# Kernel tuning notes

Hardware: AMD Instinct MI355X
Metric: run time of the kernel (lower is better)

## Reference

```python
import jax, jax.numpy as jnp
import numpy as np

C = 256          # in_channels == out_channels
L = 131072       # sequence length (multiple of BL)
BL = 64          # dilation == sliding-attention block length
CQ = C // 2      # q/k channels (r1=2)
CV = C // 2      # v channels (r2=2)
ALPHA = 1.0
EPS_IN = 1e-5    # InstanceNorm eps


def setup_inputs() -> dict:
    key = jax.random.key(0)
    ks = jax.random.split(key, 16)
    s = 0.05
    return {
        "x": jax.random.normal(ks[0], (1, C, L), jnp.float32),
        "f": jax.random.normal(ks[1], (1, C, L), jnp.float32),
        "mask": jnp.ones((1, 1, L), jnp.float32),
        # ConvFeedForward: Conv1d(C, C, 3, padding=BL, dilation=BL)
        "Wff": jax.random.normal(ks[2], (C, C, 3), jnp.float32) * s,
        "bff": jax.random.normal(ks[3], (C,), jnp.float32) * s,
        # AttLayer 1x1 convs
        "Wq": jax.random.normal(ks[4], (CQ, C), jnp.float32) * s,
        "bq": jax.random.normal(ks[5], (CQ,), jnp.float32) * s,
        "Wk": jax.random.normal(ks[6], (CQ, C), jnp.float32) * s,
        "bk": jax.random.normal(ks[7], (CQ,), jnp.float32) * s,
        "Wv": jax.random.normal(ks[8], (CV, C), jnp.float32) * s,
        "bv": jax.random.normal(ks[9], (CV,), jnp.float32) * s,
        "Wo": jax.random.normal(ks[10], (C, CV), jnp.float32) * s,
        "bo": jax.random.normal(ks[11], (C,), jnp.float32) * s,
        # AttModule.conv_1x1
        "Wc": jax.random.normal(ks[12], (C, C), jnp.float32) * s,
        "bc": jax.random.normal(ks[13], (C,), jnp.float32) * s,
    }


def _conv1x1(W, b, x):  # x: (B, Cin, L)
    return jnp.einsum('oc,bcl->bol', W, x) + b[None, :, None]


def _forward(x, f, mask, Wff, bff, Wq, bq, Wk, bk, Wv, bv, Wo, bo, Wc, bc):
    # --- ConvFeedForward: dilated conv + ReLU (same-length output) ---
    out = jax.lax.conv_general_dilated(
        x, Wff, window_strides=(1,), padding=[(BL, BL)], rhs_dilation=(BL,),
        dimension_numbers=('NCH', 'OIH', 'NCH')) + bff[None, :, None]
    out = jax.nn.relu(out)  # (1, C, L)

    # --- InstanceNorm1d (affine=False, biased var) ---
    mu = out.mean(axis=-1, keepdims=True)
    var = out.var(axis=-1, keepdims=True)
    xn = (out - mu) * jax.lax.rsqrt(var + EPS_IN)

    # --- AttLayer (sliding_att, decoder: value from f) ---
    q = _conv1x1(Wq, bq, xn)   # (1, CQ, L)
    k = _conv1x1(Wk, bk, xn)   # (1, CQ, L)
    v = _conv1x1(Wv, bv, f)    # (1, CV, L)

    nb = L // BL
    half = BL // 2
    pm = mask[:, 0:1, :]                         # (1,1,L) padding mask
    # pad halo of BL//2 zeros on each side of k, v, padding_mask
    kp = jnp.pad(k, ((0, 0), (0, 0), (half, half)))
    vp = jnp.pad(v, ((0, 0), (0, 0), (half, half)))
    mp = jnp.pad(pm, ((0, 0), (0, 0), (half, half)))
    # window index: block i sees [i*BL, i*BL + 2*BL) of the padded sequence
    idx = jnp.arange(nb)[:, None] * BL + jnp.arange(2 * BL)[None, :]  # (nb, 2BL)
    kw = kp[:, :, idx]   # (1, CQ, nb, 2BL)
    vw = vp[:, :, idx]   # (1, CV, nb, 2BL)
    mw = mp[:, 0, idx]   # (1, nb, 2BL)

    # window mask: query i attends keys [i, i+BL) within the 2BL window
    d = jnp.arange(2 * BL)[None, :] - jnp.arange(BL)[:, None]
    wm = ((d >= 0) & (d < BL)).astype(x.dtype)          # (BL, 2BL)
    fm = wm[None, None] * mw[:, :, None, :]             # (1, nb, BL, 2BL)

    qb = q.reshape(1, CQ, nb, BL)
    energy = jnp.einsum('bcnl,bcnm->bnlm', qb, kw) / np.sqrt(CQ).astype(x.dtype)
    att = jax.nn.softmax(energy + jnp.log(fm + 1e-6), axis=-1) * fm
    ov = jnp.einsum('bcnm,bnlm->bcnl', vw, att)         # (1, CV, nb, BL)
    oo = jnp.einsum('oc,bcnl->bonl', Wo, jax.nn.relu(ov)) + bo[None, :, None, None]
    att_out = oo.reshape(1, C, L) * pm                  # (1, C, L)

    # --- scaled residual + 1x1 conv + (dropout=identity) + masked residual ---
    h = ALPHA * att_out + out
    h = _conv1x1(Wc, bc, h)
    return (x + h) * mask


def reference(x, f, mask, Wff, bff, Wq, bq, Wk, bk, Wv, bv, Wo, bo, Wc, bc):
    return _forward(x, f, mask, Wff, bff, Wq, bq, Wk, bk, Wv, bv, Wo, bo, Wc, bc)
```

## Files before the change

### kernel.cpp

```cpp
#include <hip/hip_runtime.h>

#define L_LEN 131072
#define NB    2048
#define NT    1024

typedef unsigned short u16;
typedef __attribute__((ext_vector_type(4))) float f32x4;
typedef __attribute__((ext_vector_type(8))) short s16x8;
typedef __attribute__((ext_vector_type(4))) short s16x4;

#define WS_OUTT  0ull
#define WS_QT    67108864ull
#define WS_PSUM  100663296ull
#define WS_PSQ   101711872ull
#define WS_MEAN  102760448ull
#define WS_RSTD  102761472ull
#define WS_WFFB  102762496ull
#define WS_WQKB  103155712ull
#define WS_WVB   103286784ull
#define WS_WOB   103352320ull
#define WS_WCB   103417856ull
#define WS_BQKP  103548928ull

__device__ __forceinline__ u16 f2bf(float v){
  union { float f; unsigned u; } a; a.f = v;
  unsigned r = a.u + 0x7fffu + ((a.u >> 16) & 1u);
  return (u16)(r >> 16);
}
__device__ __forceinline__ float bf2f(u16 u){
  union { unsigned u; float f; } a; a.u = ((unsigned)u) << 16; return a.f;
}
__device__ __forceinline__ unsigned cvtpk(float a, float b){
  unsigned r;
  asm("v_cvt_pk_bf16_f32 %0, %1, %2" : "=v"(r) : "v"(a), "v"(b));
  return r;
}
__device__ __forceinline__ f32x4 mfma16(s16x8 a, s16x8 b, f32x4 c){
  return __builtin_amdgcn_mfma_f32_16x16x32_bf16(a, b, c, 0, 0, 0);
}
__device__ __forceinline__ s16x8 ld8(const void* p){ return *(const s16x8*)p; }

__global__ __launch_bounds__(256) void k_prep(
    const float* __restrict__ Wff, const float* __restrict__ Wv,
    const float* __restrict__ Wo,  const float* __restrict__ Wc,
    short* __restrict__ wffb, short* __restrict__ wvb,
    short* __restrict__ wob,  short* __restrict__ wcb)
{
  int i = blockIdx.x * 256 + threadIdx.x;
  if (i < 196608){
    int o = i / 768, kk = i % 768;
    int t = kk >> 8, c = kk & 255;
    wffb[i] = (short)f2bf(Wff[(o*256 + c)*3 + t]);
  } else if (i < 229376){ int j = i - 196608; wvb[j] = (short)f2bf(Wv[j]); }
  else if (i < 262144){ int j = i - 229376; wob[j] = (short)f2bf(Wo[j]); }
  else if (i < 327680){ int j = i - 262144; wcb[j] = (short)f2bf(Wc[j]); }
}

__global__ __launch_bounds__(512, 4) void k_conv(
    const float* __restrict__ x, const short* __restrict__ wffb,
    const float* __restrict__ bff, u16* __restrict__ outT,
    float* __restrict__ psum, float* __restrict__ psq)
{
  __shared__ u16 xs[2*256*40];
  const int wg = blockIdx.x, l0 = wg * 128;
  const int tid = threadIdx.x;
  const int w = tid >> 6, lane = tid & 63, p = lane & 15, g = lane >> 4;
  const int cl = tid >> 4, posq = tid & 15;

  {
    #pragma unroll
    for (int u = 0; u < 4; ++u){
      const int row = 64*u + 4*posq;
      const long gp = (long)l0 - 64 + row;
      f32x4 v = {0.f,0.f,0.f,0.f};
      if (gp >= 0 && gp + 4 <= L_LEN)
        v = *(const f32x4*)(x + (size_t)cl*L_LEN + gp);
      const unsigned r01 = cvtpk(v[0], v[1]);
      const unsigned r23 = cvtpk(v[2], v[3]);
      xs[(row+0)*40 + (cl ^ (8*(((row+0)>>2)&3)))] = (u16)(r01 & 0xffffu);
      xs[(row+1)*40 + (cl ^ (8*(((row+1)>>2)&3)))] = (u16)(r01 >> 16);
      xs[(row+2)*40 + (cl ^ (8*(((row+2)>>2)&3)))] = (u16)(r23 & 0xffffu);
      xs[(row+3)*40 + (cl ^ (8*(((row+3)>>2)&3)))] = (u16)(r23 >> 16);
    }
  }
  __syncthreads();

  f32x4 acc[2][8] = {};
  #pragma unroll 1
  for (int cg = 0; cg < 8; ++cg){
    const int cur = (cg & 1) * 10240;
    const int nxt = ((cg + 1) & 1) * 10240;
    f32x4 vv[4];
    const bool have = (cg < 7);
    if (have){
      #pragma unroll
      for (int u = 0; u < 4; ++u){
        const int row = 64*u + 4*posq;
        const long gp = (long)l0 - 64 + row;
        vv[u] = f32x4{0.f,0.f,0.f,0.f};
        if (gp >= 0 && gp + 4 <= L_LEN)
          vv[u] = *(const f32x4*)(x + (size_t)((cg+1)*32 + cl)*L_LEN + gp);
      }
    }
    #pragma unroll
    for (int t = 0; t < 3; ++t){
      s16x8 a0 = ld8(wffb + (size_t)(32*w +      p)*768 + t*256 + cg*32 + 8*g);
      s16x8 a1 = ld8(wffb + (size_t)(32*w + 16 + p)*768 + t*256 + cg*32 + 8*g);
      #pragma unroll
      for (int fn = 0; fn < 8; ++fn){
        const int row = 64*t + 16*fn + p;
        s16x8 b = ld8(&xs[cur + row*40 + ((8*g) ^ (8*((row>>2)&3)))]);
        acc[0][fn] = mfma16(a0, b, acc[0][fn]);
        acc[1][fn] = mfma16(a1, b, acc[1][fn]);
      }
    }
    if (have){
      #pragma unroll
      for (int u = 0; u < 4; ++u){
        const int row = 64*u + 4*posq;
        const unsigned r01 = cvtpk(vv[u][0], vv[u][1]);
        const unsigned r23 = cvtpk(vv[u][2], vv[u][3]);
        xs[nxt + (row+0)*40 + (cl ^ (8*(((row+0)>>2)&3)))] = (u16)(r01 & 0xffffu);
        xs[nxt + (row+1)*40 + (cl ^ (8*(((row+1)>>2)&3)))] = (u16)(r01 >> 16);
        xs[nxt + (row+2)*40 + (cl ^ (8*(((row+2)>>2)&3)))] = (u16)(r23 & 0xffffu);
        xs[nxt + (row+3)*40 + (cl ^ (8*(((row+3)>>2)&3)))] = (u16)(r23 >> 16);
      }
    }
    __syncthreads();
  }
  #pragma unroll
  for (int fm = 0; fm < 2; ++fm){
    const int o0 = 32*w + 16*fm + 4*g;
    float ssum[4] = {0,0,0,0}, ssq[4] = {0,0,0,0};
    #pragma unroll
    for (int fn = 0; fn < 8; ++fn){
      s16x4 pk;
      #pragma unroll
      for (int i = 0; i < 4; ++i){
        float val = fmaxf(acc[fm][fn][i] + bff[o0+i], 0.f);
        pk[i] = (short)f2bf(val);
        ssum[i] += val; ssq[i] += val*val;
      }
      *(s16x4*)(outT + (size_t)(l0 + 16*fn + p)*256 + o0) = pk;
    }
    #pragma unroll
    for (int i = 0; i < 4; ++i){
      float a = ssum[i], b = ssq[i];
      #pragma unroll
      for (int d = 1; d < 16; d <<= 1){ a += __shfl_xor(a, d, 16); b += __shfl_xor(b, d, 16); }
      if (p == 0){ psum[(size_t)(o0+i)*NT + wg] = a; psq[(size_t)(o0+i)*NT + wg] = b; }
    }
  }
}

__global__ __launch_bounds__(256) void k_stats(
    const float* __restrict__ psum, const float* __restrict__ psq,
    float* __restrict__ mean, float* __restrict__ rstd)
{
  __shared__ float ss[256], sq[256];
  const int ch = blockIdx.x, tid = threadIdx.x;
  float a = 0.f, b = 0.f;
  for (int j = tid; j < NT; j += 256){ a += psum[(size_t)ch*NT + j]; b += psq[(size_t)ch*NT + j]; }
  ss[tid] = a; sq[tid] = b;
  __syncthreads();
  for (int st = 128; st > 0; st >>= 1){
    if (tid < st){ ss[tid] += ss[tid+st]; sq[tid] += sq[tid+st]; }
    __syncthreads();
  }
  if (tid == 0){
    float m = ss[0] / (float)L_LEN;
    float v = sq[0] / (float)L_LEN - m*m;
    mean[ch] = m;
    rstd[ch] = rsqrtf(v + 1e-5f);
  }
}

__global__ __launch_bounds__(256) void k_adj(
    const float* __restrict__ Wq, const float* __restrict__ Wk,
    const float* __restrict__ bq, const float* __restrict__ bk,
    const float* __restrict__ mean, const float* __restrict__ rstd,
    short* __restrict__ wqkb, float* __restrict__ bqkp)
{
  __shared__ float red[256];
  const int o = blockIdx.x, c = threadIdx.x;
  const float* src = (o < 128) ? (Wq + (size_t)o*256) : (Wk + (size_t)(o-128)*256);
  const float bias = (o < 128) ? bq[o] : bk[o-128];
  float wv = src[c] * rstd[c];
  wqkb[o*256 + c] = (short)f2bf(wv);
  red[c] = wv * mean[c];
  __syncthreads();
  for (int st = 128; st > 0; st >>= 1){
    if (c < st) red[c] += red[c+st];
    __syncthreads();
  }
  if (c == 0) bqkp[o] = bias - red[0];
}

__global__ __launch_bounds__(256, 4) void k_v(
    const float* __restrict__ fin, const short* __restrict__ wvb,
    const float* __restrict__ bv, u16* __restrict__ vout)
{
  __shared__ u16 xs[2*128*40];
  const int wg = blockIdx.x, l0 = wg * 128;
  const int tid = threadIdx.x;
  const int w = tid >> 6, lane = tid & 63, p = lane & 15, g = lane >> 4;
  const int cl = tid >> 3, posq = tid & 7;

  {
    #pragma unroll
    for (int u = 0; u < 4; ++u){
      const int row = 32*u + 4*posq;
      f32x4 v = *(const f32x4*)(fin + (size_t)cl*L_LEN + l0 + row);
      const unsigned r01 = cvtpk(v[0], v[1]);
      const unsigned r23 = cvtpk(v[2], v[3]);
      xs[(row+0)*40 + (cl ^ (8*(((row+0)>>2)&3)))] = (u16)(r01 & 0xffffu);
      xs[(row+1)*40 + (cl ^ (8*(((row+1)>>2)&3)))] = (u16)(r01 >> 16);
      xs[(row+2)*40 + (cl ^ (8*(((row+2)>>2)&3)))] = (u16)(r23 & 0xffffu);
      xs[(row+3)*40 + (cl ^ (8*(((row+3)>>2)&3)))] = (u16)(r23 >> 16);
    }
  }
  __syncthreads();

  f32x4 acc[2][8] = {};
  #pragma unroll 1
  for (int cg = 0; cg < 8; ++cg){
    const int cur = (cg & 1) * 5120;
    const int nxt = ((cg + 1) & 1) * 5120;
    f32x4 vv[4];
    const bool have = (cg < 7);
    if (have){
      #pragma unroll
      for (int u = 0; u < 4; ++u){
        const int row = 32*u + 4*posq;
        vv[u] = *(const f32x4*)(fin + (size_t)((cg+1)*32 + cl)*L_LEN + l0 + row);
      }
    }
    s16x8 af[2];
    af[0] = ld8(wvb + (size_t)(32*w +      p)*256 + cg*32 + 8*g);
    af[1] = ld8(wvb + (size_t)(32*w + 16 + p)*256 + cg*32 + 8*g);
    #pragma unroll
    for (int fn = 0; fn < 8; ++fn){
      const int row = 16*fn + p;
      s16x8 b = ld8(&xs[cur + row*40 + ((8*g) ^ (8*((row>>2)&3)))]);
      acc[0][fn] = mfma16(af[0], b, acc[0][fn]);
      acc[1][fn] = mfma16(af[1], b, acc[1][fn]);
    }
    if (have){
      #pragma unroll
      for (int u = 0; u < 4; ++u){
        const int row = 32*u + 4*posq;
        const unsigned r01 = cvtpk(vv[u][0], vv[u][1]);
        const unsigned r23 = cvtpk(vv[u][2], vv[u][3]);
        xs[nxt + (row+0)*40 + (cl ^ (8*(((row+0)>>2)&3)))] = (u16)(r01 & 0xffffu);
        xs[nxt + (row+1)*40 + (cl ^ (8*(((row+1)>>2)&3)))] = (u16)(r01 >> 16);
        xs[nxt + (row+2)*40 + (cl ^ (8*(((row+2)>>2)&3)))] = (u16)(r23 & 0xffffu);
        xs[nxt + (row+3)*40 + (cl ^ (8*(((row+3)>>2)&3)))] = (u16)(r23 >> 16);
      }
    }
    __syncthreads();
  }
  #pragma unroll
  for (int fm = 0; fm < 2; ++fm){
    #pragma unroll
    for (int fn = 0; fn < 8; ++fn){
      #pragma unroll
      for (int i = 0; i < 4; ++i){
        const int cv = 32*w + 16*fm + 4*g + i;
        vout[(size_t)cv*L_LEN + l0 + 16*fn + p] = f2bf(acc[fm][fn][i] + bv[cv]);
      }
    }
  }
}

__global__ __launch_bounds__(512, 4) void k_qk(
    const u16* __restrict__ outT, const short* __restrict__ wqkb,
    const float* __restrict__ bqkp, u16* __restrict__ qT, u16* __restrict__ kT)
{
  extern __shared__ u16 tile[];
  const int wg = blockIdx.x, l0 = wg * 128;
  const int tid = threadIdx.x;
  const int w = tid >> 6, lane = tid & 63, p = lane & 15, g = lane >> 4;
  #pragma unroll
  for (int rep = 0; rep < 8; ++rep){
    const int idx = rep*512 + tid;
    const int r = idx >> 5, cc = idx & 31;
    s16x8 vput = ld8(outT + (size_t)(l0 + r)*256 + cc*8);
    *(s16x8*)(&tile[r*256 + ((cc*8) ^ ((r&7)<<3))]) = vput;
  }
  __syncthreads();
  f32x4 acc[2][8] = {};
  #pragma unroll
  for (int kk = 0; kk < 8; ++kk){
    s16x8 af[2];
    af[0] = ld8(wqkb + (size_t)(32*w +      p)*256 + 32*kk + 8*g);
    af[1] = ld8(wqkb + (size_t)(32*w + 16 + p)*256 + 32*kk + 8*g);
    #pragma unroll
    for (int fn = 0; fn < 8; ++fn){
      const int r = 16*fn + p;
      s16x8 b = ld8(&tile[r*256 + ((32*kk + 8*g) ^ ((r&7)<<3))]);
      acc[0][fn] = mfma16(af[0], b, acc[0][fn]);
      acc[1][fn] = mfma16(af[1], b, acc[1][fn]);
    }
  }
  #pragma unroll
  for (int fm = 0; fm < 2; ++fm){
    const int R0 = 32*w + 16*fm + 4*g;
    #pragma unroll
    for (int fn = 0; fn < 8; ++fn){
      s16x4 pk;
      #pragma unroll
      for (int i = 0; i < 4; ++i) pk[i] = (short)f2bf(acc[fm][fn][i] + bqkp[R0+i]);
      const size_t row = (size_t)(l0 + 16*fn + p);
      if (R0 < 128) *(s16x4*)(qT + row*128 + R0)       = pk;
      else          *(s16x4*)(kT + row*128 + R0 - 128) = pk;
    }
  }
}

__global__ __launch_bounds__(256, 4) void k_attn(
    const u16* __restrict__ qT, const u16* __restrict__ kT,
    const u16* __restrict__ vg, const short* __restrict__ wob,
    const float* __restrict__ bo, const float* __restrict__ mask,
    u16* __restrict__ outT)
{
  __shared__ u16 klds[16384];
  __shared__ float maskw[128];
  const int tid = threadIdx.x;
  const int w = tid >> 6, lane = tid & 63, p = lane & 15, g = lane >> 4;
  const int n = blockIdx.x, s = n * 64;
  const float SCALE = 0.08838834764831845f;

  #pragma unroll
  for (int rep = 0; rep < 8; ++rep){
    const int idx = rep*256 + tid;
    const int m = idx >> 4, cc = idx & 15;
    const int gpos = s - 32 + m;
    s16x8 vput = {};
    if (gpos >= 0 && gpos < L_LEN) vput = ld8(kT + (size_t)gpos*128 + cc*8);
    *(s16x8*)(&klds[m*128 + ((cc*8) ^ ((m&7)<<3))]) = vput;
  }
  if (tid < 128){
    const int gp = s - 32 + tid;
    maskw[tid] = (gp >= 0 && gp < L_LEN) ? mask[gp] : 0.f;
  }
  __syncthreads();

  f32x4 e[8] = {};
  #pragma unroll
  for (int kk = 0; kk < 4; ++kk){
    s16x8 aq = ld8(qT + (size_t)(s + 16*w + p)*128 + 32*kk + 8*g);
    #pragma unroll
    for (int fn = 0; fn < 8; ++fn){
      const int m = 16*fn + p;
      s16x8 b = ld8(&klds[m*128 + ((32*kk + 8*g) ^ ((m&7)<<3))]);
      e[fn] = mfma16(aq, b, e[fn]);
    }
  }
  float M[4] = {-1e30f,-1e30f,-1e30f,-1e30f};
  float S[4] = {0.f,0.f,0.f,0.f};
  #pragma unroll
  for (int fn = 0; fn < 8; ++fn){
    #pragma unroll
    for (int i = 0; i < 4; ++i){
      const int mm = 16*fn + p;
      const int l_ = 16*w + 4*g + i;
      const int d = mm - l_;
      const float fmv = (d >= 0 && d < 64) ? maskw[mm] : 0.f;
      const float z = e[fn][i]*SCALE + __logf(fmv + 1e-6f);
      e[fn][i] = z;
      M[i] = fmaxf(M[i], z);
    }
  }
  #pragma unroll
  for (int i = 0; i < 4; ++i){
    #pragma unroll
    for (int d = 1; d < 16; d <<= 1) M[i] = fmaxf(M[i], __shfl_xor(M[i], d, 16));
  }
  #pragma unroll
  for (int fn = 0; fn < 8; ++fn){
    #pragma unroll
    for (int i = 0; i < 4; ++i){
      const float pv = __expf(e[fn][i] - M[i]);
      e[fn][i] = pv;
      S[i] += pv;
    }
  }
  #pragma unroll
  for (int i = 0; i < 4; ++i){
    #pragma unroll
    for (int d = 1; d < 16; d <<= 1) S[i] += __shfl_xor(S[i], d, 16);
  }
  float rinv[4];
  #pragma unroll
  for (int i = 0; i < 4; ++i) rinv[i] = 1.f / S[i];
  __syncthreads();
  #pragma unroll
  for (int fn = 0; fn < 8; ++fn){
    #pragma unroll
    for (int i = 0; i < 4; ++i){
      const int mm = 16*fn + p;
      const int l_ = 16*w + 4*g + i;
      const int d = mm - l_;
      const float fmv = (d >= 0 && d < 64) ? maskw[mm] : 0.f;
      klds[l_*128 + (mm ^ ((l_&7)<<3))] = f2bf(e[fn][i] * rinv[i] * fmv);
    }
  }
  __syncthreads();

  f32x4 accp[2][4] = {};
  #pragma unroll
  for (int kk = 0; kk < 4; ++kk){
    int gp0 = s - 32 + 32*kk + 8*g;
    gp0 = max(0, min(gp0, L_LEN - 8));
    s16x8 a0 = ld8(vg + (size_t)(32*w +      p)*L_LEN + gp0);
    s16x8 a1 = ld8(vg + (size_t)(32*w + 16 + p)*L_LEN + gp0);
    #pragma unroll
    for (int fn = 0; fn < 4; ++fn){
      const int l_ = 16*fn + p;
      s16x8 b = ld8(&klds[l_*128 + ((32*kk + 8*g) ^ ((l_&7)<<3))]);
      accp[0][fn] = mfma16(a0, b, accp[0][fn]);
      accp[1][fn] = mfma16(a1, b, accp[1][fn]);
    }
  }
  #pragma unroll
  for (int fm = 0; fm < 2; ++fm){
    #pragma unroll
    for (int fn = 0; fn < 4; ++fn){
      const int l_ = 16*fn + p;
      s16x4 pk;
      #pragma unroll
      for (int i = 0; i < 4; ++i) pk[i] = (short)f2bf(fmaxf(accp[fm][fn][i], 0.f));
      const int cv0 = 32*w + 16*fm + 4*g;
      *(s16x4*)(&klds[8192 + l_*128 + (cv0 ^ ((l_&7)<<3))]) = pk;
    }
  }
  __syncthreads();

  f32x4 acco[4][4] = {};
  #pragma unroll
  for (int kk = 0; kk < 4; ++kk){
    s16x8 a[4];
    #pragma unroll
    for (int fm = 0; fm < 4; ++fm)
      a[fm] = ld8(wob + (size_t)(64*w + 16*fm + p)*128 + 32*kk + 8*g);
    #pragma unroll
    for (int fn = 0; fn < 4; ++fn){
      const int l_ = 16*fn + p;
      s16x8 b = ld8(&klds[8192 + l_*128 + ((32*kk + 8*g) ^ ((l_&7)<<3))]);
      #pragma unroll
      for (int fm = 0; fm < 4; ++fm) acco[fm][fn] = mfma16(a[fm], b, acco[fm][fn]);
    }
  }
  #pragma unroll
  for (int fm = 0; fm < 4; ++fm){
    const int o0 = 64*w + 16*fm + 4*g;
    #pragma unroll
    for (int fn = 0; fn < 4; ++fn){
      const int l_ = 16*fn + p;
      const float pml = maskw[32 + l_];
      u16* hp = outT + (size_t)(s + l_)*256 + o0;
      s16x4 res = *(const s16x4*)hp;
      s16x4 pk;
      #pragma unroll
      for (int i = 0; i < 4; ++i){
        float hv = (acco[fm][fn][i] + bo[o0+i]) * pml + bf2f((u16)res[i]);
        pk[i] = (short)f2bf(hv);
      }
      *(s16x4*)hp = pk;
    }
  }
}

__global__ __launch_bounds__(512, 4) void k_wc(
    const u16* __restrict__ hT, const short* __restrict__ wcb,
    const float* __restrict__ bc, const float* __restrict__ x,
    const float* __restrict__ mask, float* __restrict__ dout)
{
  extern __shared__ u16 tile[];
  const int wg = blockIdx.x, l0 = wg * 128;
  const int tid = threadIdx.x;
  const int w = tid >> 6, lane = tid & 63, p = lane & 15, g = lane >> 4;
  #pragma unroll
  for (int rep = 0; rep < 8; ++rep){
    const int idx = rep*512 + tid;
    const int r = idx >> 5, cc = idx & 31;
    s16x8 vput = ld8(hT + (size_t)(l0 + r)*256 + cc*8);
    *(s16x8*)(&tile[r*256 + ((cc*8) ^ ((r&7)<<3))]) = vput;
  }
  __syncthreads();
  f32x4 acc[2][8] = {};
  #pragma unroll
  for (int kk = 0; kk < 8; ++kk){
    s16x8 af[2];
    af[0] = ld8(wcb + (size_t)(32*w +      p)*256 + 32*kk + 8*g);
    af[1] = ld8(wcb + (size_t)(32*w + 16 + p)*256 + 32*kk + 8*g);
    #pragma unroll
    for (int fn = 0; fn < 8; ++fn){
      const int r = 16*fn + p;
      s16x8 b = ld8(&tile[r*256 + ((32*kk + 8*g) ^ ((r&7)<<3))]);
      acc[0][fn] = mfma16(af[0], b, acc[0][fn]);
      acc[1][fn] = mfma16(af[1], b, acc[1][fn]);
    }
  }
  #pragma unroll
  for (int fm = 0; fm < 2; ++fm){
    const int o0 = 32*w + 16*fm + 4*g;
    #pragma unroll
    for (int fn = 0; fn < 8; ++fn){
      const int pos = l0 + 16*fn + p;
      const float mk = mask[pos];
      #pragma unroll
      for (int i = 0; i < 4; ++i){
        const size_t idx = (size_t)(o0+i)*L_LEN + pos;
        dout[idx] = (x[idx] + acc[fm][fn][i] + bc[o0+i]) * mk;
      }
    }
  }
}

extern "C" void kernel_launch(void* const* d_in, const int* in_sizes, int n_in,
                              void* d_out, int out_size, void* d_ws, size_t ws_size,
                              hipStream_t stream)
{
  (void)in_sizes; (void)n_in; (void)out_size; (void)ws_size;
  const float* x    = (const float*)d_in[0];
  const float* f    = (const float*)d_in[1];
  const float* mask = (const float*)d_in[2];
  const float* Wff  = (const float*)d_in[3];
  const float* bff  = (const float*)d_in[4];
  const float* Wq   = (const float*)d_in[5];
  const float* bq   = (const float*)d_in[6];
  const float* Wk   = (const float*)d_in[7];
  const float* bk   = (const float*)d_in[8];
  const float* Wv   = (const float*)d_in[9];
  const float* bv   = (const float*)d_in[10];
  const float* Wo   = (const float*)d_in[11];
  const float* bo   = (const float*)d_in[12];
  const float* Wc   = (const float*)d_in[13];
  const float* bc   = (const float*)d_in[14];

  char* ws = (char*)d_ws;
  u16*   outT = (u16*)(ws + WS_OUTT);
  u16*   qT   = (u16*)(ws + WS_QT);
  float* psum = (float*)(ws + WS_PSUM);
  float* psq  = (float*)(ws + WS_PSQ);
  float* mean = (float*)(ws + WS_MEAN);
  float* rstd = (float*)(ws + WS_RSTD);
  short* wffb = (short*)(ws + WS_WFFB);
  short* wqkb = (short*)(ws + WS_WQKB);
  short* wvb  = (short*)(ws + WS_WVB);
  short* wob  = (short*)(ws + WS_WOB);
  short* wcb  = (short*)(ws + WS_WCB);
  float* bqkp = (float*)(ws + WS_BQKP);

  u16* vbuf = (u16*)d_out;
  u16* ktb  = (u16*)((char*)d_out + 33554432);

  (void)hipFuncSetAttribute((const void*)k_qk,
                            hipFuncAttributeMaxDynamicSharedMemorySize, 65536);
  (void)hipFuncSetAttribute((const void*)k_wc,
                            hipFuncAttributeMaxDynamicSharedMemorySize, 65536);

  k_prep <<<1280, 256, 0, stream>>>(Wff, Wv, Wo, Wc, wffb, wvb, wob, wcb);
  k_conv <<<NT,   512, 0, stream>>>(x, wffb, bff, outT, psum, psq);
  k_stats<<<256,  256, 0, stream>>>(psum, psq, mean, rstd);
  k_adj  <<<256,  256, 0, stream>>>(Wq, Wk, bq, bk, mean, rstd, wqkb, bqkp);
  k_v    <<<NT,   256, 0, stream>>>(f, wvb, bv, vbuf);
  k_qk   <<<NT,   512, 65536, stream>>>(outT, wqkb, bqkp, qT, ktb);
  k_attn <<<NB,   256, 0, stream>>>(qT, ktb, vbuf, wob, bo, mask, outT);
  k_wc   <<<NT,   512, 65536, stream>>>(outT, wcb, bc, x, mask, (float*)d_out);
}
```

Before: 405.5 us.

## Split conv output channels across two blocks and widen k_v to 512 threads

The dilated-conv kernel now launches 2048 blocks, with each block computing half of the output channels for a 128-position tile. Its 8 waves are arranged as 4 channel groups times 2 position halves, and per-channel partial statistics from the two position halves are combined in shared memory. The value projection kernel moves to 512 threads, so each wave computes 16 output channels instead of 32. The intent is more parallelism and fewer accumulator registers per wave for higher occupancy. The cost is that each x tile is loaded and converted twice in the conv, plus an extra shared-memory reduction step.

```diff
diff --git a/kernel.cpp b/kernel.cpp
--- a/kernel.cpp
+++ b/kernel.cpp
@@ -62,9 +62,13 @@
     float* __restrict__ psum, float* __restrict__ psq)
 {
   __shared__ u16 xs[2*256*40];
-  const int wg = blockIdx.x, l0 = wg * 128;
+  const int bid = blockIdx.x;
+  const int oh = (bid >> 3) & 1;
+  const int pt = ((bid >> 4) << 3) | (bid & 7);
+  const int l0 = pt * 128;
   const int tid = threadIdx.x;
   const int w = tid >> 6, lane = tid & 63, p = lane & 15, g = lane >> 4;
+  const int wo = w >> 1, wp = w & 1;
   const int cl = tid >> 4, posq = tid & 15;
 
   {
@@ -85,7 +89,7 @@
   }
   __syncthreads();
 
-  f32x4 acc[2][8] = {};
+  f32x4 acc[2][4] = {};
   #pragma unroll 1
   for (int cg = 0; cg < 8; ++cg){
     const int cur = (cg & 1) * 10240;
@@ -104,11 +108,11 @@
     }
     #pragma unroll
     for (int t = 0; t < 3; ++t){
-      s16x8 a0 = ld8(wffb + (size_t)(32*w +      p)*768 + t*256 + cg*32 + 8*g);
-      s16x8 a1 = ld8(wffb + (size_t)(32*w + 16 + p)*768 + t*256 + cg*32 + 8*g);
-      #pragma unroll
-      for (int fn = 0; fn < 8; ++fn){
-        const int row = 64*t + 16*fn + p;
+      s16x8 a0 = ld8(wffb + (size_t)(128*oh + 32*wo +      p)*768 + t*256 + cg*32 + 8*g);
+      s16x8 a1 = ld8(wffb + (size_t)(128*oh + 32*wo + 16 + p)*768 + t*256 + cg*32 + 8*g);
+      #pragma unroll
+      for (int fn = 0; fn < 4; ++fn){
+        const int row = 64*t + 64*wp + 16*fn + p;
         s16x8 b = ld8(&xs[cur + row*40 + ((8*g) ^ (8*((row>>2)&3)))]);
         acc[0][fn] = mfma16(a0, b, acc[0][fn]);
         acc[1][fn] = mfma16(a1, b, acc[1][fn]);
@@ -128,27 +132,58 @@
     }
     __syncthreads();
   }
+
+  float* sred = (float*)xs;
+  float ssum[2][4], ssq[2][4];
   #pragma unroll
   for (int fm = 0; fm < 2; ++fm){
-    const int o0 = 32*w + 16*fm + 4*g;
-    float ssum[4] = {0,0,0,0}, ssq[4] = {0,0,0,0};
-    #pragma unroll
-    for (int fn = 0; fn < 8; ++fn){
+    const int ol = 32*wo + 16*fm + 4*g;
+    #pragma unroll
+    for (int i = 0; i < 4; ++i){ ssum[fm][i] = 0.f; ssq[fm][i] = 0.f; }
+    #pragma unroll
+    for (int fn = 0; fn < 4; ++fn){
+      const int pos = l0 + 64*wp + 16*fn + p;
       s16x4 pk;
       #pragma unroll
       for (int i = 0; i < 4; ++i){
-        float val = fmaxf(acc[fm][fn][i] + bff[o0+i], 0.f);
+        float val = fmaxf(acc[fm][fn][i] + bff[128*oh + ol + i], 0.f);
         pk[i] = (short)f2bf(val);
-        ssum[i] += val; ssq[i] += val*val;
-      }
-      *(s16x4*)(outT + (size_t)(l0 + 16*fn + p)*256 + o0) = pk;
+        ssum[fm][i] += val; ssq[fm][i] += val*val;
+      }
+      *(s16x4*)(outT + (size_t)pos*256 + 128*oh + ol) = pk;
     }
     #pragma unroll
     for (int i = 0; i < 4; ++i){
-      float a = ssum[i], b = ssq[i];
-      #pragma unroll
-      for (int d = 1; d < 16; d <<= 1){ a += __shfl_xor(a, d, 16); b += __shfl_xor(b, d, 16); }
-      if (p == 0){ psum[(size_t)(o0+i)*NT + wg] = a; psq[(size_t)(o0+i)*NT + wg] = b; }
+      #pragma unroll
+      for (int d = 1; d < 16; d <<= 1){
+        ssum[fm][i] += __shfl_xor(ssum[fm][i], d, 16);
+        ssq[fm][i]  += __shfl_xor(ssq[fm][i],  d, 16);
+      }
+    }
+  }
+  __syncthreads();
+  if (wp == 1 && p == 0){
+    #pragma unroll
+    for (int fm = 0; fm < 2; ++fm){
+      const int ol = 32*wo + 16*fm + 4*g;
+      #pragma unroll
+      for (int i = 0; i < 4; ++i){
+        sred[(ol+i)*2+0] = ssum[fm][i];
+        sred[(ol+i)*2+1] = ssq[fm][i];
+      }
+    }
+  }
+  __syncthreads();
+  if (wp == 0 && p == 0){
+    #pragma unroll
+    for (int fm = 0; fm < 2; ++fm){
+      const int ol = 32*wo + 16*fm + 4*g;
+      #pragma unroll
+      for (int i = 0; i < 4; ++i){
+        const int og = 128*oh + ol + i;
+        psum[(size_t)og*NT + pt] = ssum[fm][i] + sred[(ol+i)*2+0];
+        psq [(size_t)og*NT + pt] = ssq[fm][i]  + sred[(ol+i)*2+1];
+      }
     }
   }
 }
@@ -196,7 +231,7 @@
   if (c == 0) bqkp[o] = bias - red[0];
 }
 
-__global__ __launch_bounds__(256, 4) void k_v(
+__global__ __launch_bounds__(512, 4) void k_v(
     const float* __restrict__ fin, const short* __restrict__ wvb,
     const float* __restrict__ bv, u16* __restrict__ vout)
 {
@@ -204,12 +239,12 @@
   const int wg = blockIdx.x, l0 = wg * 128;
   const int tid = threadIdx.x;
   const int w = tid >> 6, lane = tid & 63, p = lane & 15, g = lane >> 4;
-  const int cl = tid >> 3, posq = tid & 7;
+  const int cl = tid >> 4, posq = tid & 15;
 
   {
     #pragma unroll
-    for (int u = 0; u < 4; ++u){
-      const int row = 32*u + 4*posq;
+    for (int u = 0; u < 2; ++u){
+      const int row = 8*posq + 4*u;
       f32x4 v = *(const f32x4*)(fin + (size_t)cl*L_LEN + l0 + row);
       const unsigned r01 = cvtpk(v[0], v[1]);
       const unsigned r23 = cvtpk(v[2], v[3]);
@@ -221,34 +256,31 @@
   }
   __syncthreads();
 
-  f32x4 acc[2][8] = {};
+  f32x4 acc[8] = {};
   #pragma unroll 1
   for (int cg = 0; cg < 8; ++cg){
     const int cur = (cg & 1) * 5120;
     const int nxt = ((cg + 1) & 1) * 5120;
-    f32x4 vv[4];
+    f32x4 vv[2];
     const bool have = (cg < 7);
     if (have){
       #pragma unroll
-      for (int u = 0; u < 4; ++u){
-        const int row = 32*u + 4*posq;
+      for (int u = 0; u < 2; ++u){
+        const int row = 8*posq + 4*u;
         vv[u] = *(const f32x4*)(fin + (size_t)((cg+1)*32 + cl)*L_LEN + l0 + row);
       }
     }
-    s16x8 af[2];
-    af[0] = ld8(wvb + (size_t)(32*w +      p)*256 + cg*32 + 8*g);
-    af[1] = ld8(wvb + (size_t)(32*w + 16 + p)*256 + cg*32 + 8*g);
+    s16x8 af = ld8(wvb + (size_t)(16*w + p)*256 + cg*32 + 8*g);
     #pragma unroll
     for (int fn = 0; fn < 8; ++fn){
       const int row = 16*fn + p;
       s16x8 b = ld8(&xs[cur + row*40 + ((8*g) ^ (8*((row>>2)&3)))]);
-      acc[0][fn] = mfma16(af[0], b, acc[0][fn]);
-      acc[1][fn] = mfma16(af[1], b, acc[1][fn]);
+      acc[fn] = mfma16(af, b, acc[fn]);
     }
     if (have){
       #pragma unroll
-      for (int u = 0; u < 4; ++u){
-        const int row = 32*u + 4*posq;
+      for (int u = 0; u < 2; ++u){
+        const int row = 8*posq + 4*u;
         const unsigned r01 = cvtpk(vv[u][0], vv[u][1]);
         const unsigned r23 = cvtpk(vv[u][2], vv[u][3]);
         xs[nxt + (row+0)*40 + (cl ^ (8*(((row+0)>>2)&3)))] = (u16)(r01 & 0xffffu);
@@ -260,14 +292,11 @@
     __syncthreads();
   }
   #pragma unroll
-  for (int fm = 0; fm < 2; ++fm){
-    #pragma unroll
-    for (int fn = 0; fn < 8; ++fn){
-      #pragma unroll
-      for (int i = 0; i < 4; ++i){
-        const int cv = 32*w + 16*fm + 4*g + i;
-        vout[(size_t)cv*L_LEN + l0 + 16*fn + p] = f2bf(acc[fm][fn][i] + bv[cv]);
-      }
+  for (int fn = 0; fn < 8; ++fn){
+    #pragma unroll
+    for (int i = 0; i < 4; ++i){
+      const int cv = 16*w + 4*g + i;
+      vout[(size_t)cv*L_LEN + l0 + 16*fn + p] = f2bf(acc[fn][i] + bv[cv]);
     }
   }
 }
@@ -562,10 +591,10 @@
                             hipFuncAttributeMaxDynamicSharedMemorySize, 65536);
 
   k_prep <<<1280, 256, 0, stream>>>(Wff, Wv, Wo, Wc, wffb, wvb, wob, wcb);
-  k_conv <<<NT,   512, 0, stream>>>(x, wffb, bff, outT, psum, psq);
+  k_conv <<<2048, 512, 0, stream>>>(x, wffb, bff, outT, psum, psq);
   k_stats<<<256,  256, 0, stream>>>(psum, psq, mean, rstd);
   k_adj  <<<256,  256, 0, stream>>>(Wq, Wk, bq, bk, mean, rstd, wqkb, bqkp);
-  k_v    <<<NT,   256, 0, stream>>>(f, wvb, bv, vbuf);
+  k_v    <<<NT,   512, 0, stream>>>(f, wvb, bv, vbuf);
   k_qk   <<<NT,   512, 65536, stream>>>(outT, wqkb, bqkp, qT, ktb);
   k_attn <<<NB,   256, 0, stream>>>(qT, ktb, vbuf, wob, bo, mask, outT);
   k_wc   <<<NT,   512, 65536, stream>>>(outT, wcb, bc, x, mask, (float*)d_out);
```

Result: no change. 409.7 us (+1.0%).
